# Optimization experiments

Measured on AMD Instinct MI355X. Metric: run time of the kernel, lower is better.

The kernel has to match this reference:

```python
import jax, jax.numpy as jnp
import numpy as np
from jax import lax


def _ln(x, g, b, eps=1e-5):
    m = jnp.mean(x, axis=-1, keepdims=True)
    v = jnp.mean((x - m) ** 2, axis=-1, keepdims=True)
    return (x - m) / jnp.sqrt(v + eps) * g + b


def _lin(x, w, b):  # torch Linear: w [out,in]
    return x @ w.T + b


def _conv(x, w, b, stride, pad):
    y = lax.conv_general_dilated(x, w, (stride, stride), pad,
                                 dimension_numbers=('NCHW', 'OIHW', 'NCHW'))
    return y + b[None, :, None, None]


def _haar_dwt(x):
    # J=1 haar, zero mode, even H/W: per 2x2 block [[a,b],[c,d]]
    a = x[:, :, 0::2, 0::2]
    bb = x[:, :, 0::2, 1::2]
    c = x[:, :, 1::2, 0::2]
    d = x[:, :, 1::2, 1::2]
    ll = (a + bb + c + d) * 0.5
    lohi = (a - bb + c - d) * 0.5  # band 0 (col-high)
    hilo = (a + bb - c - d) * 0.5  # band 1 (row-high)
    hihi = (a - bb - c + d) * 0.5  # band 2
    return ll, lohi, hilo, hihi


def _cross_attention(q, k, v):
    # q,k,v: [b, d, c]; 8 equal chunks along d; softmax over QUERY axis (torch dim=1)
    b, d, c = q.shape
    chunk = d // 8
    qc = q.reshape(b, 8, chunk, c)
    kc = k.reshape(b, 8, chunk, c)
    vc = v.reshape(b, 8, chunk, c)
    att = jnp.einsum('bnqc,bnkc->bnqk', qc, kc) * (8.0 ** -0.5)
    att = jax.nn.softmax(att, axis=2)  # normalize over q (matches F.softmax dim=1)
    out = jnp.einsum('bnqk,bnkc->bnqc', att, vc)
    return out.reshape(b, d, c)


def _ffn(x, ln1_g, ln1_b, fc1_w, fc1_b, div_w, div_b, fc2_w, fc2_b,
         ln3_g, ln3_b, fc3a_w, fc3a_b, fc3b_w, fc3b_b, lnn_g, lnn_b, act_w, act_b):
    x1 = jax.nn.gelu(_lin(_ln(x, ln1_g, ln1_b), fc1_w, fc1_b), approximate=False)
    x2 = jax.nn.gelu(_lin(x, div_w, div_b), approximate=False) - x1
    x2 = jax.nn.gelu(_lin(x2, fc2_w, fc2_b), approximate=False)
    x3 = _lin(jax.nn.gelu(_lin(_ln(x, ln3_g, ln3_b), fc3a_w, fc3a_b), approximate=False), fc3b_w, fc3b_b)
    gate = jax.nn.sigmoid(_lin(x, act_w, act_b))
    # dropout(0.5) is identity in eval mode
    return gate * _ln(x2 + x3, lnn_g, lnn_b)


def _resize_bilinear_ac(x, oh, ow):
    # bilinear, align_corners=True
    B, C, H, W = x.shape
    def idx(n_in, n_out):
        pos = jnp.linspace(0.0, n_in - 1.0, n_out)
        i0 = jnp.floor(pos).astype(jnp.int32)
        i1 = jnp.minimum(i0 + 1, n_in - 1)
        return i0, i1, (pos - i0).astype(x.dtype)
    y0, y1, wy = idx(H, oh)
    x0, x1, wx = idx(W, ow)
    r = x[:, :, y0, :] * (1 - wy)[None, None, :, None] + x[:, :, y1, :] * wy[None, None, :, None]
    return r[:, :, :, x0] * (1 - wx)[None, None, None, :] + r[:, :, :, x1] * wx[None, None, None, :]


def setup_inputs() -> dict:
    key = jax.random.key(0)
    ks = jax.random.split(key, 25)
    B, Cin, H, W = 16, 128, 128, 128
    Ch = 128  # out_planes // 2
    def nrm(k, shp, s=0.02):
        return jax.random.normal(k, shp, jnp.float32) * s
    inp = {
        'x': jax.random.normal(ks[0], (B, Cin, H, W), jnp.float32),
        'conv1_w': nrm(ks[1], (Ch, 2 * Cin, 1, 1)), 'conv1_b': jnp.zeros((Ch,), jnp.float32),
        'l1_w': nrm(ks[2], (Ch, Cin, 4, 4)), 'l1_b': jnp.zeros((Ch,), jnp.float32),
        'ln1_g': jnp.ones((Ch,), jnp.float32), 'ln1_b': jnp.zeros((Ch,), jnp.float32),
        'fc1_w': nrm(ks[3], (Ch, Ch)), 'fc1_b': jnp.zeros((Ch,), jnp.float32),
        'div_w': nrm(ks[4], (Ch, Ch)), 'div_b': jnp.zeros((Ch,), jnp.float32),
        'fc2_w': nrm(ks[5], (Ch, Ch)), 'fc2_b': jnp.zeros((Ch,), jnp.float32),
        'ln3_g': jnp.ones((Ch,), jnp.float32), 'ln3_b': jnp.zeros((Ch,), jnp.float32),
        'fc3a_w': nrm(ks[6], (Ch, Ch)), 'fc3a_b': jnp.zeros((Ch,), jnp.float32),
        'fc3b_w': nrm(ks[7], (Ch, Ch)), 'fc3b_b': jnp.zeros((Ch,), jnp.float32),
        'lnn_g': jnp.ones((Ch,), jnp.float32), 'lnn_b': jnp.zeros((Ch,), jnp.float32),
        'act_w': nrm(ks[8], (Ch, Ch)), 'act_b': jnp.zeros((Ch,), jnp.float32),
    }
    return inp


def reference(x, conv1_w, conv1_b, l1_w, l1_b, ln1_g, ln1_b, fc1_w, fc1_b,
              div_w, div_b, fc2_w, fc2_b, ln3_g, ln3_b, fc3a_w, fc3a_b,
              fc3b_w, fc3b_b, lnn_g, lnn_b, act_w, act_b):
    dw = jax.nn.relu(_conv(x, l1_w, l1_b, 2, ((1, 1), (1, 1))))
    yL, y_HL, y_LH, y_HH = _haar_dwt(x)
    y = _conv(jnp.concatenate((y_HL, y_LH), axis=1), conv1_w, conv1_b, 1, ((0, 0), (0, 0)))
    b, c, h, w = y.shape
    y_t = y.transpose(0, 2, 3, 1).reshape(b, h * w, c)
    yL_t = yL.transpose(0, 2, 3, 1).reshape(b, h * w, c)
    yHH_t = y_HH.transpose(0, 2, 3, 1).reshape(b, h * w, c)
    att = _cross_attention(yL_t, y_t, yHH_t)
    att = _ffn(att, ln1_g, ln1_b, fc1_w, fc1_b, div_w, div_b, fc2_w, fc2_b,
               ln3_g, ln3_b, fc3a_w, fc3a_b, fc3b_w, fc3b_b, lnn_g, lnn_b, act_w, act_b)
    att = att.reshape(b, h, w, c).transpose(0, 3, 1, 2)
    y_img = y_t.reshape(b, h, w, c).transpose(0, 3, 1, 2)
    down_2x = _resize_bilinear_ac(x, h, w)
    att = att * (down_2x - dw)
    return att + y_img
```

## Files before the change

kernel.cpp:

```cpp
#include <hip/hip_runtime.h>
#include <cmath>


#define EPI_NONE 0
#define EPI_GELU 1
#define EPI_GELU_SUB 2
#define EPI_ADD 3
#define EPI_SIGMOID 4
#define EPI_EXP 5

typedef unsigned short u16;
typedef __bf16 v8bf __attribute__((ext_vector_type(8)));
typedef float f32x4 __attribute__((ext_vector_type(4)));

__device__ __forceinline__ float gelu_f(float v) {
  return 0.5f * v * (1.f + erff(v * 0.70710678118654752f));
}
__device__ __forceinline__ float sigmoid_f(float v) {
  return 1.f / (1.f + __expf(-v));
}
__device__ __forceinline__ float bf2f(u16 h) {
  return __uint_as_float((unsigned)h << 16);
}
__device__ __forceinline__ u16 f2bf(float f) {
  unsigned u = __float_as_uint(f);
  return (u16)((u + 0x7fffu + ((u >> 16) & 1u)) >> 16);
}
__device__ __forceinline__ unsigned f2bf_pk(float lo, float hi) {
  unsigned a = __float_as_uint(lo), b = __float_as_uint(hi);
  a = (a + 0x7fffu + ((a >> 16) & 1u)) >> 16;
  b = (b + 0x7fffu + ((b >> 16) & 1u)) >> 16;
  return a | (b << 16);
}
__device__ __forceinline__ void gld_lds16(const void* g, void* l) {
  __builtin_amdgcn_global_load_lds(
      (const __attribute__((address_space(1))) unsigned int*)g,
      (__attribute__((address_space(3))) unsigned int*)l, 16, 0, 0);
}

__global__ __launch_bounds__(256) void pre_k(const float* __restrict__ x,
                                             u16* __restrict__ yL16,
                                             u16* __restrict__ yHHt16,
                                             u16* __restrict__ hllh16,
                                             u16* __restrict__ xpt) {
  int gx = blockIdx.x;
  int jt = gx & 1, cit = gx >> 1;
  int i = blockIdx.y, b = blockIdx.z;
  int j0 = jt * 32, ci0 = cit * 32;
  int tx = threadIdx.x & 31, ty = threadIdx.x >> 5;
  __shared__ float sll[32][33], shl[32][33], slh[32][33], shh[32][33];
  if (gx == 0) {
    int pl = 1 + ((threadIdx.x >> 7) << 1);
    long off = ((long)(b * 4 + pl) * 4160 + (long)i * 65) * 128 + (threadIdx.x & 127);
    xpt[off] = 0;
  } else if (gx == 1) {
    int pl = (threadIdx.x >> 7) << 1;
    long off = ((long)(b * 4 + pl) * 4160 + (long)i * 65 + 64) * 128 + (threadIdx.x & 127);
    xpt[off] = 0;
  }
  const float2* x2 = (const float2*)x;
#pragma unroll
  for (int k = 0; k < 4; ++k) {
    int ci = ty + 8 * k;
    long base = (((long)b * 128 + ci0 + ci) * 128 + 2 * i) * 64 + j0 + tx;
    float2 ab = x2[base];
    float2 cd = x2[base + 64];
    float a = ab.x, bb = ab.y, c = cd.x, d = cd.y;
    sll[ci][tx] = (a + bb + c + d) * 0.5f;
    shl[ci][tx] = (a - bb + c - d) * 0.5f;
    slh[ci][tx] = (a + bb - c - d) * 0.5f;
    shh[ci][tx] = (a - bb - c + d) * 0.5f;
  }
  __syncthreads();
  long tok = (long)b * 4096 + i * 64 + j0;
  int r = threadIdx.x >> 3;
  int q4 = (threadIdx.x & 7) << 2;
  float vll[4], vhl[4], vlh[4], vhh[4];
#pragma unroll
  for (int e = 0; e < 4; ++e) {
    vll[e] = sll[q4 + e][r];
    vhl[e] = shl[q4 + e][r];
    vlh[e] = slh[q4 + e][r];
    vhh[e] = shh[q4 + e][r];
  }
  uint2 u;
  u.x = f2bf_pk(vll[0], vll[1]);
  u.y = f2bf_pk(vll[2], vll[3]);
  *(uint2*)(yL16 + (tok + r) * 128 + ci0 + q4) = u;
  u.x = f2bf_pk(vhl[0], vhl[1]);
  u.y = f2bf_pk(vhl[2], vhl[3]);
  *(uint2*)(hllh16 + (tok + r) * 256 + ci0 + q4) = u;
  u.x = f2bf_pk(vlh[0], vlh[1]);
  u.y = f2bf_pk(vlh[2], vlh[3]);
  *(uint2*)(hllh16 + (tok + r) * 256 + 128 + ci0 + q4) = u;
  {
    int ch = threadIdx.x >> 3;
    int t4 = (threadIdx.x & 7) << 2;
    uint2 h;
    h.x = f2bf_pk(shh[ch][t4], shh[ch][t4 + 1]);
    h.y = f2bf_pk(shh[ch][t4 + 2], shh[ch][t4 + 3]);
    *(uint2*)(yHHt16 + (long)(ci0 + ch) * 65536 + tok + t4) = h;
  }
  {
    long rb = (long)(b * 4) * 4160 + (long)i * 65;
    int ci = j0 + r;
    float pA[4], pB[4], pC[4], pD[4];
#pragma unroll
    for (int e = 0; e < 4; ++e) {
      pA[e] = 0.5f * (vll[e] + vhl[e] + vlh[e] + vhh[e]);
      pB[e] = 0.5f * (vll[e] - vhl[e] + vlh[e] - vhh[e]);
      pC[e] = 0.5f * (vll[e] + vhl[e] - vlh[e] - vhh[e]);
      pD[e] = 0.5f * (vll[e] - vhl[e] - vlh[e] + vhh[e]);
    }
    u.x = f2bf_pk(pA[0], pA[1]);
    u.y = f2bf_pk(pA[2], pA[3]);
    *(uint2*)(xpt + (rb + ci) * 128 + ci0 + q4) = u;
    u.x = f2bf_pk(pB[0], pB[1]);
    u.y = f2bf_pk(pB[2], pB[3]);
    *(uint2*)(xpt + (rb + 4160 + ci + 1) * 128 + ci0 + q4) = u;
    u.x = f2bf_pk(pC[0], pC[1]);
    u.y = f2bf_pk(pC[2], pC[3]);
    *(uint2*)(xpt + (rb + 8320 + ci) * 128 + ci0 + q4) = u;
    u.x = f2bf_pk(pD[0], pD[1]);
    u.y = f2bf_pk(pD[2], pD[3]);
    *(uint2*)(xpt + (rb + 12480 + ci + 1) * 128 + ci0 + q4) = u;
  }
}

__global__ __launch_bounds__(256) void wcvt8_k(
    const float* __restrict__ a0, const float* __restrict__ a1,
    const float* __restrict__ a2, const float* __restrict__ a3,
    const float* __restrict__ a4, const float* __restrict__ a5,
    const float* __restrict__ a6, const float* __restrict__ a7,
    unsigned* __restrict__ dst, unsigned* __restrict__ zp) {
  if (blockIdx.x >= 768) {
    zp[(blockIdx.x - 768) * 256 + threadIdx.x] = 0;
    return;
  }
  int f = blockIdx.x * 256 + threadIdx.x;
  int e = 2 * f;
  if (e < 262144) {
    int ch = e >> 13, kg = (e >> 10) & 7, n = (e >> 3) & 127, ke = e & 7;
    int k = ch * 64 + kg * 8 + ke;
    int stg = ch >> 2, sub = ch & 3;
    int kwsel = sub >> 1, chalf = sub & 1;
    int kh = stg >> 1, cp = stg & 1;
    int kw = cp ? (kwsel ? 2 : 0) : (kwsel ? 3 : 1);
    int c = chalf * 64 + (k & 63);
    long si = (((long)n * 128 + c) * 4 + kh) * 4 + kw;
    dst[f] = f2bf_pk(a0[si], a0[si + 16]);
    return;
  }
  const float* s; int b;
  if (e < 294912)      { s = a1; b = 262144; }
  else if (e < 311296) { s = a2; b = 294912; }
  else if (e < 327680) { s = a3; b = 311296; }
  else if (e < 344064) { s = a4; b = 327680; }
  else if (e < 360448) { s = a5; b = 344064; }
  else if (e < 376832) { s = a6; b = 360448; }
  else                 { s = a7; b = 376832; }
  dst[f] = f2bf_pk(s[e - b], s[e - b + 1]);
}

template <int AMODE, int EPI>
__global__ __launch_bounds__(256) void gemm16_k(
    const u16* __restrict__ A, long sA, int lda,
    const u16* __restrict__ B, long sB, int ldb,
    u16* __restrict__ C, long sC, int ldc,
    int K, float alpha, const float* __restrict__ bias,
    const u16* __restrict__ aux, const float* __restrict__ sc) {
  __shared__ __align__(16) char smem[32768];
  char* As = smem;
  char* Bs = smem + 16384;
  int z = blockIdx.z;
  int tid = threadIdx.x, lane = tid & 63, w = tid >> 6;
  int wm = w >> 1, wn = w & 1, l15 = lane & 15, l4 = lane >> 4;
  const u16* Ab = A + (long)z * sA + (long)blockIdx.x * 128 * lda;
  const u16* Bb = B + (long)z * sB + (long)blockIdx.y * 128 * ldb;
  const float* scz = (AMODE == 1) ? sc + (long)z * K : nullptr;
  int sm = tid >> 3, skg = tid & 7;
  int sbase = sm * 128 + ((skg ^ (sm & 7)) << 4);
  uint4 pa[4], pb[4];

  auto loadAB = [&](int k0) {
#pragma unroll
    for (int u = 0; u < 4; ++u) {
      pb[u] = *(const uint4*)(Bb + (long)(sm + 32 * u) * ldb + k0 + skg * 8);
      uint4 v = *(const uint4*)(Ab + (long)(sm + 32 * u) * lda + k0 + skg * 8);
      if (AMODE == 1) {
        float4 s0 = *(const float4*)(scz + k0 + skg * 8);
        float4 s1 = *(const float4*)(scz + k0 + skg * 8 + 4);
        v.x = f2bf_pk(bf2f((u16)(v.x & 0xffff)) * s0.x, bf2f((u16)(v.x >> 16)) * s0.y);
        v.y = f2bf_pk(bf2f((u16)(v.y & 0xffff)) * s0.z, bf2f((u16)(v.y >> 16)) * s0.w);
        v.z = f2bf_pk(bf2f((u16)(v.z & 0xffff)) * s1.x, bf2f((u16)(v.z >> 16)) * s1.y);
        v.w = f2bf_pk(bf2f((u16)(v.w & 0xffff)) * s1.z, bf2f((u16)(v.w >> 16)) * s1.w);
      }
      pa[u] = v;
    }
  };

  f32x4 acc[4][4] = {};
  loadAB(0);
  int nch = K >> 6;
  for (int ch = 0; ch < nch; ++ch) {
    __syncthreads();
#pragma unroll
    for (int u = 0; u < 4; ++u) {
      *(uint4*)(As + sbase + u * 4096) = pa[u];
      *(uint4*)(Bs + sbase + u * 4096) = pb[u];
    }
    __syncthreads();
    if (ch + 1 < nch) loadAB((ch + 1) << 6);
#pragma unroll
    for (int s = 0; s < 2; ++s) {
      int ko = (((s << 2) | l4) ^ (l15 & 7)) << 4;
      v8bf af[4], bfr[4];
#pragma unroll
      for (int t = 0; t < 4; ++t) {
        af[t] = *(const v8bf*)(As + (64 * wm + 16 * t + l15) * 128 + ko);
        bfr[t] = *(const v8bf*)(Bs + (64 * wn + 16 * t + l15) * 128 + ko);
      }
#pragma unroll
      for (int mt = 0; mt < 4; ++mt)
#pragma unroll
        for (int nt = 0; nt < 4; ++nt)
          acc[mt][nt] = __builtin_amdgcn_mfma_f32_16x16x32_bf16(af[mt], bfr[nt], acc[mt][nt], 0, 0, 0);
    }
  }
  u16* Cb = C + (long)z * sC;
#pragma unroll
  for (int mt = 0; mt < 4; ++mt) {
#pragma unroll
    for (int nt = 0; nt < 4; ++nt) {
      f32x4 a = acc[mt][nt];
      int n = blockIdx.y * 128 + 64 * wn + 16 * nt + l15;
      float bv = bias ? bias[n] : 0.f;
#pragma unroll
      for (int r = 0; r < 4; ++r) {
        long m = (long)blockIdx.x * 128 + 64 * wm + 16 * mt + 4 * l4 + r;
        float v = a[r] * alpha + bv;
        if (EPI == EPI_GELU) v = gelu_f(v);
        else if (EPI == EPI_GELU_SUB) v = gelu_f(v) - bf2f(aux[m * ldc + n]);
        else if (EPI == EPI_ADD) v += bf2f(aux[m * ldc + n]);
        else if (EPI == EPI_SIGMOID) v = sigmoid_f(v);
        else if (EPI == EPI_EXP) v = __expf(v);
        Cb[m * ldc + n] = f2bf(v);
      }
    }
  }
}

__global__ __launch_bounds__(256) __attribute__((amdgpu_waves_per_eu(4)))
void conv4g_k(const u16* __restrict__ xpt, const u16* __restrict__ wb,
              const float* __restrict__ bias, const u16* __restrict__ zp,
              u16* __restrict__ dw16) {
  __shared__ __align__(16) char smem[33280];
  char* As = smem;
  int raw = blockIdx.x;
  int swz = (raw & 7) * 128 + (raw >> 3);
  int oi = swz & 63, b = swz >> 6;
  int tid = threadIdx.x, lane = tid & 63, w = tid >> 6;
  int wm = w >> 1, wn = w & 1, l15 = lane & 15, l4 = lane >> 4;
  f32x4 acc[2][4] = {};

  auto issueA = [&](int stg2, int bsel) {
    int kh = stg2 >> 1, cp2 = stg2 & 1;
    int roff = (kh == 0) ? -1 : (kh == 3) ? 1 : 0;
    int ri = oi + roff;
    int ph = (((kh + 1) & 1) << 1) | cp2;
    const u16* rowb = ((unsigned)ri < 64u)
        ? xpt + ((long)(b * 4 + ph) * 4160 + (long)ri * 65) * 128
        : zp;
    char* lb = As + bsel * 16640 + w * 1024;
#pragma unroll
    for (int i = 0; i < 4; ++i) {
      int d = i * 4096 + w * 1024 + lane * 16;
      int slot = d >> 8, cg = (d >> 4) & 15;
      gld_lds16(rowb + slot * 128 + ((cg ^ ((slot - cp2) & 7)) << 3),
                lb + i * 4096);
    }
    if (tid < 16) {
      gld_lds16(rowb + 64 * 128 + ((lane ^ ((64 - cp2) & 7)) << 3),
                As + bsel * 16640 + 16384);
    }
  };

  issueA(0, 0);
  for (int stg = 0; stg < 8; ++stg) {
    __syncthreads();
    if (stg < 7) issueA(stg + 1, (stg + 1) & 1);
    const char* Ab = As + (stg & 1) * 16640;
    int cp2 = stg & 1;
#pragma unroll
    for (int sub = 0; sub < 4; ++sub) {
      int chunk = stg * 4 + sub;
      const int kwsel = sub >> 1, chalf = sub & 1;
#pragma unroll
      for (int s = 0; s < 2; ++s) {
        v8bf bw[4], af[2];
#pragma unroll
        for (int nt = 0; nt < 4; ++nt) {
          int row = 64 * wn + 16 * nt + l15;
          bw[nt] = *(const v8bf*)(wb + ((long)(chunk * 8 + s * 4 + l4) * 128 + row) * 8);
        }
#pragma unroll
        for (int mt = 0; mt < 2; ++mt) {
          int slot = 32 * wm + 16 * mt + l15 + kwsel;
          int cg = chalf * 8 + s * 4 + l4;
          af[mt] = *(const v8bf*)(Ab + slot * 256 + ((cg ^ ((slot - cp2) & 7)) << 4));
        }
#pragma unroll
        for (int mt = 0; mt < 2; ++mt)
#pragma unroll
          for (int nt = 0; nt < 4; ++nt)
            acc[mt][nt] = __builtin_amdgcn_mfma_f32_16x16x32_bf16(
                af[mt], bw[nt], acc[mt][nt], 0, 0, 0);
      }
    }
  }
  __syncthreads();
  float* buf = (float*)(smem + w * 2176);
  long obase = ((long)b * 128) * 4096 + oi * 64;
#pragma unroll
  for (int cg = 0; cg < 4; ++cg) {
    int co = 64 * wn + 16 * cg + l15;
    float bv = bias[co];
#pragma unroll
    for (int mt = 0; mt < 2; ++mt) {
      f32x4 a = acc[mt][cg];
#pragma unroll
      for (int r = 0; r < 4; ++r)
        buf[l15 * 34 + 16 * mt + 4 * l4 + r] = fmaxf(a[r] + bv, 0.f);
    }
    __syncthreads();
#pragma unroll
    for (int it = 0; it < 8; ++it) {
      int row = it * 2 + (lane >> 5);
      int mcol = lane & 31;
      int coz = 64 * wn + 16 * cg + row;
      dw16[obase + (long)coz * 4096 + 32 * wm + mcol] = f2bf(buf[row * 34 + mcol]);
    }
    __syncthreads();
  }
}

__global__ __launch_bounds__(256) void ssum_k(const u16* __restrict__ E,
                                              float* __restrict__ sc) {
  int z = blockIdx.y;
  int k = blockIdx.x * 256 + threadIdx.x;
  const u16* Eb = E + (long)z * 262144 + k;
  float s = 0.f;
#pragma unroll 8
  for (int q = 0; q < 512; ++q) s += bf2f(Eb[(long)q * 512]);
  sc[(long)z * 512 + k] = 1.f / s;
}

__global__ __launch_bounds__(256) void ln16_k(const u16* __restrict__ X,
                                              const float* __restrict__ g,
                                              const float* __restrict__ bt,
                                              const u16* __restrict__ gate,
                                              u16* __restrict__ Y) {
  int t = (blockIdx.x * 256 + threadIdx.x) >> 6;
  int lane = threadIdx.x & 63;
  const u16* xr = X + (long)t * 128;
  float v0 = bf2f(xr[lane]), v1 = bf2f(xr[lane + 64]);
  float s = v0 + v1, sq = v0 * v0 + v1 * v1;
#pragma unroll
  for (int off = 32; off > 0; off >>= 1) {
    s += __shfl_xor(s, off);
    sq += __shfl_xor(sq, off);
  }
  float mean = s * 0.0078125f;
  float var = sq * 0.0078125f - mean * mean;
  float rstd = rsqrtf(var + 1e-5f);
  float y0 = (v0 - mean) * rstd * g[lane] + bt[lane];
  float y1 = (v1 - mean) * rstd * g[lane + 64] + bt[lane + 64];
  if (gate) {
    y0 *= bf2f(gate[(long)t * 128 + lane]);
    y1 *= bf2f(gate[(long)t * 128 + lane + 64]);
  }
  Y[(long)t * 128 + lane] = f2bf(y0);
  Y[(long)t * 128 + lane + 64] = f2bf(y1);
}

__global__ __launch_bounds__(256) void combine_k(const u16* __restrict__ attf,
                                                 const u16* __restrict__ yt,
                                                 const u16* __restrict__ dw16,
                                                 const float* __restrict__ x,
                                                 float* __restrict__ out) {
  int gx = blockIdx.x;
  int jt = gx & 1, cot = gx >> 1;
  int i = blockIdx.y, b = blockIdx.z;
  int j0 = jt * 32, co0 = cot * 32;
  int tx = threadIdx.x & 31, ty = threadIdx.x >> 5;
  __shared__ float sa[32][33], sy[32][33];
  long tokbase = (long)b * 4096 + i * 64 + j0;
#pragma unroll
  for (int k = 0; k < 4; ++k) {
    int row = ty + 8 * k;
    long idx = (tokbase + row) * 128 + co0 + tx;
    sa[row][tx] = bf2f(attf[idx]);
    sy[row][tx] = bf2f(yt[idx]);
  }
  __syncthreads();
  float py = (float)(i * 127) / 63.0f;
  int y0 = (int)py;
  int y1 = min(y0 + 1, 127);
  float wy = py - (float)y0;
  int j = j0 + tx;
  float px = (float)(j * 127) / 63.0f;
  int x0 = (int)px;
  int x1 = min(x0 + 1, 127);
  float wx = px - (float)x0;
#pragma unroll
  for (int k = 0; k < 4; ++k) {
    int co = co0 + ty + 8 * k;
    const float* xb = x + (((long)b * 128 + co) * 128) * 128;
    float r0 = xb[y0 * 128 + x0] * (1.f - wx) + xb[y0 * 128 + x1] * wx;
    float r1 = xb[y1 * 128 + x0] * (1.f - wx) + xb[y1 * 128 + x1] * wx;
    float d2 = r0 * (1.f - wy) + r1 * wy;
    long oidx = (((long)b * 128 + co) * 64 + i) * 64 + j;
    float dwv = bf2f(dw16[oidx]);
    out[oidx] = sa[tx][ty + 8 * k] * (d2 - dwv) + sy[tx][ty + 8 * k];
  }
}

extern "C" void kernel_launch(void* const* d_in, const int* in_sizes, int n_in,
                              void* d_out, int out_size, void* d_ws, size_t ws_size,
                              hipStream_t stream) {
  const float* x = (const float*)d_in[0];
  const float* w1 = (const float*)d_in[1];
  const float* b1 = (const float*)d_in[2];
  const float* l1w = (const float*)d_in[3];
  const float* l1b = (const float*)d_in[4];
  const float* ln1g = (const float*)d_in[5];
  const float* ln1b = (const float*)d_in[6];
  const float* fc1w = (const float*)d_in[7];
  const float* fc1b = (const float*)d_in[8];
  const float* divw = (const float*)d_in[9];
  const float* divb = (const float*)d_in[10];
  const float* fc2w = (const float*)d_in[11];
  const float* fc2b = (const float*)d_in[12];
  const float* ln3g = (const float*)d_in[13];
  const float* ln3b = (const float*)d_in[14];
  const float* fc3aw = (const float*)d_in[15];
  const float* fc3ab = (const float*)d_in[16];
  const float* fc3bw = (const float*)d_in[17];
  const float* fc3bb = (const float*)d_in[18];
  const float* lnng = (const float*)d_in[19];
  const float* lnnb = (const float*)d_in[20];
  const float* actw = (const float*)d_in[21];
  const float* actb = (const float*)d_in[22];

  char* W = (char*)d_ws;
  u16* yL16 = (u16*)(W);
  u16* hllh16 = (u16*)(W + 16777216L);
  u16* yHHt16 = (u16*)(W + 50331648L);
  u16* y16 = (u16*)(W + 67108864L);
  u16* S16 = (u16*)(W + 83886080L);
  u16* attO16 = (u16*)(W + 150994944L);
  u16* dw16 = (u16*)(W + 167772160L);
  u16* t1 = (u16*)(W + 184549376L);
  u16* t2 = (u16*)(W + 201326592L);
  u16* t3 = (u16*)(W + 218103808L);
  u16* t4 = (u16*)(W + 234881024L);
  float* sc = (float*)(W + 251658240L);
  u16* wall = (u16*)(W + 251920384L);
  u16* l1wb = wall;
  u16* w1b = wall + 262144;
  u16* fc1b16 = wall + 294912;
  u16* divb16 = wall + 311296;
  u16* fc2b16 = wall + 327680;
  u16* fc3ab16 = wall + 344064;
  u16* fc3bb16 = wall + 360448;
  u16* actb16 = wall + 376832;
  u16* xpt16 = S16;
  u16* zp16 = (u16*)(W + 152043520L);

  dim3 blk(256);
  const float qk_scale = 0.35355339059327373f;

  wcvt8_k<<<dim3(785), blk, 0, stream>>>(l1w, w1, fc1w, divw, fc2w, fc3aw,
                                         fc3bw, actw, (unsigned*)wall,
                                         (unsigned*)zp16);
  pre_k<<<dim3(8, 64, 16), blk, 0, stream>>>(x, yL16, yHHt16, hllh16, xpt16);
  gemm16_k<0, EPI_NONE><<<dim3(512, 1, 1), blk, 0, stream>>>(
      hllh16, 0, 256, w1b, 0, 256, y16, 0, 128, 256, 1.f, b1, nullptr, nullptr);
  conv4g_k<<<dim3(1024), blk, 0, stream>>>(xpt16, l1wb, l1b, zp16, dw16);
  gemm16_k<0, EPI_EXP><<<dim3(4, 4, 128), blk, 0, stream>>>(
      yL16, 65536, 128, y16, 65536, 128, S16, 262144, 512, 128, qk_scale,
      nullptr, nullptr, nullptr);
  ssum_k<<<dim3(2, 128), blk, 0, stream>>>(S16, sc);
  gemm16_k<1, EPI_NONE><<<dim3(4, 1, 128), blk, 0, stream>>>(
      S16, 262144, 512, yHHt16, 512, 65536, attO16, 65536, 128, 512, 1.f,
      nullptr, nullptr, sc);
  ln16_k<<<16384, blk, 0, stream>>>(attO16, ln1g, ln1b, nullptr, t1);
  gemm16_k<0, EPI_GELU><<<dim3(512, 1, 1), blk, 0, stream>>>(
      t1, 0, 128, fc1b16, 0, 128, t2, 0, 128, 128, 1.f, fc1b, nullptr, nullptr);
  gemm16_k<0, EPI_GELU_SUB><<<dim3(512, 1, 1), blk, 0, stream>>>(
      attO16, 0, 128, divb16, 0, 128, t3, 0, 128, 128, 1.f, divb, t2, nullptr);
  gemm16_k<0, EPI_GELU><<<dim3(512, 1, 1), blk, 0, stream>>>(
      t3, 0, 128, fc2b16, 0, 128, t4, 0, 128, 128, 1.f, fc2b, nullptr, nullptr);
  ln16_k<<<16384, blk, 0, stream>>>(attO16, ln3g, ln3b, nullptr, t1);
  gemm16_k<0, EPI_GELU><<<dim3(512, 1, 1), blk, 0, stream>>>(
      t1, 0, 128, fc3ab16, 0, 128, t3, 0, 128, 128, 1.f, fc3ab, nullptr, nullptr);
  gemm16_k<0, EPI_ADD><<<dim3(512, 1, 1), blk, 0, stream>>>(
      t3, 0, 128, fc3bb16, 0, 128, t1, 0, 128, 128, 1.f, fc3bb, t4, nullptr);
  gemm16_k<0, EPI_SIGMOID><<<dim3(512, 1, 1), blk, 0, stream>>>(
      attO16, 0, 128, actb16, 0, 128, t3, 0, 128, 128, 1.f, actb, nullptr, nullptr);
  ln16_k<<<16384, blk, 0, stream>>>(t1, lnng, lnnb, t3, t2);
  combine_k<<<dim3(8, 64, 16), blk, 0, stream>>>(t2, y16, dw16, x, (float*)d_out);
}
```

Before: 663.4 us.

## Fuse entire FFN block (layernorms, six GEMMs, epilogues) into one kernel

Replaces nine separate launches (three layernorm kernels and six small GEMMs with epilogues) with a single kernel. Each block loads a 64-token tile into LDS and runs every layernorm, matmul and activation on chip. Only the final gated layernorm output goes back to global memory. This removes the round trips of intermediate activations through HBM and the launch overhead. In exchange it adds many block-wide barriers, reads weights straight from global or cache in every block, and runs with lower per-block GEMM parallelism.

Result: faster. 610.0 us (-8.0%).

```diff
diff --git a/kernel.cpp b/kernel.cpp
--- a/kernel.cpp
+++ b/kernel.cpp
@@ -3,10 +3,6 @@
 
 
 #define EPI_NONE 0
-#define EPI_GELU 1
-#define EPI_GELU_SUB 2
-#define EPI_ADD 3
-#define EPI_SIGMOID 4
 #define EPI_EXP 5
 
 typedef unsigned short u16;
@@ -239,13 +235,184 @@
       for (int r = 0; r < 4; ++r) {
         long m = (long)blockIdx.x * 128 + 64 * wm + 16 * mt + 4 * l4 + r;
         float v = a[r] * alpha + bv;
-        if (EPI == EPI_GELU) v = gelu_f(v);
-        else if (EPI == EPI_GELU_SUB) v = gelu_f(v) - bf2f(aux[m * ldc + n]);
-        else if (EPI == EPI_ADD) v += bf2f(aux[m * ldc + n]);
-        else if (EPI == EPI_SIGMOID) v = sigmoid_f(v);
-        else if (EPI == EPI_EXP) v = __expf(v);
+        if (EPI == EPI_EXP) v = __expf(v);
         Cb[m * ldc + n] = f2bf(v);
       }
+    }
+  }
+}
+
+__global__ __launch_bounds__(256) void ffn_k(
+    const u16* __restrict__ Xg,
+    const u16* __restrict__ w_fc1, const u16* __restrict__ w_div,
+    const u16* __restrict__ w_fc2, const u16* __restrict__ w_fc3a,
+    const u16* __restrict__ w_fc3b, const u16* __restrict__ w_act,
+    const float* __restrict__ b_fc1, const float* __restrict__ b_div,
+    const float* __restrict__ b_fc2, const float* __restrict__ b_fc3a,
+    const float* __restrict__ b_fc3b, const float* __restrict__ b_act,
+    const float* __restrict__ ln1g, const float* __restrict__ ln1b,
+    const float* __restrict__ ln3g, const float* __restrict__ ln3b,
+    const float* __restrict__ lnng, const float* __restrict__ lnnb,
+    u16* __restrict__ out) {
+  __shared__ __align__(16) char smem[49152];
+  char* X = smem;
+  char* A = smem + 16384;
+  char* E = smem + 32768;
+  int z = blockIdx.x;
+  long t0 = (long)z * 64;
+  int tid = threadIdx.x, lane = tid & 63, w = tid >> 6;
+  int wm = w >> 1, wn = w & 1, l15 = lane & 15, l4 = lane >> 4;
+
+  {
+    const u16* src = Xg + t0 * 128;
+#pragma unroll
+    for (int r = 0; r < 4; ++r) {
+      int u = r * 256 + tid;
+      int row = u >> 4, cg = u & 15;
+      gld_lds16(src + row * 128 + ((cg ^ (row & 7)) << 3),
+                X + (r * 256 + w * 64) * 16);
+    }
+  }
+
+  auto gemm = [&](const char* Asrc, const u16* Bg, f32x4 (&acc)[2][4]) {
+#pragma unroll
+    for (int mt = 0; mt < 2; ++mt)
+#pragma unroll
+      for (int nt = 0; nt < 4; ++nt) acc[mt][nt] = f32x4{0.f, 0.f, 0.f, 0.f};
+#pragma unroll
+    for (int s = 0; s < 4; ++s) {
+      v8bf af[2], bw[4];
+#pragma unroll
+      for (int mt = 0; mt < 2; ++mt) {
+        int row = 32 * wm + 16 * mt + l15;
+        af[mt] = *(const v8bf*)(Asrc + row * 256 + (((s * 4 + l4) ^ (row & 7)) << 4));
+      }
+#pragma unroll
+      for (int nt = 0; nt < 4; ++nt) {
+        int rn = 64 * wn + 16 * nt + l15;
+        bw[nt] = *(const v8bf*)(Bg + rn * 128 + (s * 4 + l4) * 8);
+      }
+#pragma unroll
+      for (int mt = 0; mt < 2; ++mt)
+#pragma unroll
+        for (int nt = 0; nt < 4; ++nt)
+          acc[mt][nt] = __builtin_amdgcn_mfma_f32_16x16x32_bf16(
+              af[mt], bw[nt], acc[mt][nt], 0, 0, 0);
+    }
+  };
+
+  auto epi = [&](f32x4 (&acc)[2][4], const float* bias, char* dst,
+                 const char* Eb, int mode) {
+#pragma unroll
+    for (int nt = 0; nt < 4; ++nt) {
+      int n = 64 * wn + 16 * nt + l15;
+      float bv = bias[n];
+#pragma unroll
+      for (int mt = 0; mt < 2; ++mt) {
+#pragma unroll
+        for (int r = 0; r < 4; ++r) {
+          int m = 32 * wm + 16 * mt + 4 * l4 + r;
+          int off = m * 256 + (((n >> 3) ^ (m & 7)) << 4) + (n & 7) * 2;
+          float v = acc[mt][nt][r] + bv;
+          if (mode == 0) v = gelu_f(v);
+          else if (mode == 1) v = gelu_f(v) - bf2f(*(const u16*)(Eb + off));
+          else if (mode == 2) v += bf2f(*(const u16*)(Eb + off));
+          else v = sigmoid_f(v);
+          *(u16*)(dst + off) = f2bf(v);
+        }
+      }
+    }
+  };
+
+  auto lnpass = [&](const char* src, char* dst, const float* g,
+                    const float* bt) {
+    int row = w * 16 + (lane >> 2), q = lane & 3;
+    float v[32];
+    float s = 0.f, sq = 0.f;
+#pragma unroll
+    for (int gi = 0; gi < 4; ++gi) {
+      int gr = q * 4 + gi;
+      v8bf hv = *(const v8bf*)(src + row * 256 + ((gr ^ (row & 7)) << 4));
+#pragma unroll
+      for (int e = 0; e < 8; ++e) {
+        float f = bf2f(((const u16*)&hv)[e]);
+        v[gi * 8 + e] = f;
+        s += f;
+        sq += f * f;
+      }
+    }
+    s += __shfl_xor(s, 1); sq += __shfl_xor(sq, 1);
+    s += __shfl_xor(s, 2); sq += __shfl_xor(sq, 2);
+    float mean = s * 0.0078125f;
+    float rstd = rsqrtf(sq * 0.0078125f - mean * mean + 1e-5f);
+#pragma unroll
+    for (int gi = 0; gi < 4; ++gi) {
+      int gr = q * 4 + gi;
+      int c0 = gr * 8;
+      unsigned o[4];
+#pragma unroll
+      for (int e = 0; e < 4; ++e) {
+        float y0 = (v[gi * 8 + 2 * e] - mean) * rstd * g[c0 + 2 * e] + bt[c0 + 2 * e];
+        float y1 = (v[gi * 8 + 2 * e + 1] - mean) * rstd * g[c0 + 2 * e + 1] + bt[c0 + 2 * e + 1];
+        o[e] = f2bf_pk(y0, y1);
+      }
+      *(uint4*)(dst + row * 256 + ((gr ^ (row & 7)) << 4)) = *(uint4*)o;
+    }
+  };
+
+  f32x4 acc[2][4];
+  __syncthreads();
+  lnpass(X, A, ln1g, ln1b); __syncthreads();
+  gemm(A, w_fc1, acc); __syncthreads();
+  epi(acc, b_fc1, E, nullptr, 0); __syncthreads();
+  gemm(X, w_div, acc); __syncthreads();
+  epi(acc, b_div, A, E, 1); __syncthreads();
+  gemm(A, w_fc2, acc); __syncthreads();
+  epi(acc, b_fc2, E, nullptr, 0); __syncthreads();
+  lnpass(X, A, ln3g, ln3b); __syncthreads();
+  gemm(A, w_fc3a, acc); __syncthreads();
+  epi(acc, b_fc3a, A, nullptr, 0); __syncthreads();
+  gemm(A, w_fc3b, acc); __syncthreads();
+  epi(acc, b_fc3b, A, E, 2); __syncthreads();
+  gemm(X, w_act, acc); __syncthreads();
+  epi(acc, b_act, E, nullptr, 3); __syncthreads();
+
+  {
+    int row = w * 16 + (lane >> 2), q = lane & 3;
+    float v[32];
+    float s = 0.f, sq = 0.f;
+#pragma unroll
+    for (int gi = 0; gi < 4; ++gi) {
+      int gr = q * 4 + gi;
+      v8bf hv = *(const v8bf*)(A + row * 256 + ((gr ^ (row & 7)) << 4));
+#pragma unroll
+      for (int e = 0; e < 8; ++e) {
+        float f = bf2f(((const u16*)&hv)[e]);
+        v[gi * 8 + e] = f;
+        s += f;
+        sq += f * f;
+      }
+    }
+    s += __shfl_xor(s, 1); sq += __shfl_xor(sq, 1);
+    s += __shfl_xor(s, 2); sq += __shfl_xor(sq, 2);
+    float mean = s * 0.0078125f;
+    float rstd = rsqrtf(sq * 0.0078125f - mean * mean + 1e-5f);
+    u16* og = out + (t0 + row) * 128;
+#pragma unroll
+    for (int gi = 0; gi < 4; ++gi) {
+      int gr = q * 4 + gi;
+      int c0 = gr * 8;
+      v8bf gv = *(const v8bf*)(E + row * 256 + ((gr ^ (row & 7)) << 4));
+      unsigned o[4];
+#pragma unroll
+      for (int e = 0; e < 4; ++e) {
+        float y0 = ((v[gi * 8 + 2 * e] - mean) * rstd * lnng[c0 + 2 * e] + lnnb[c0 + 2 * e]) *
+                   bf2f(((const u16*)&gv)[2 * e]);
+        float y1 = ((v[gi * 8 + 2 * e + 1] - mean) * rstd * lnng[c0 + 2 * e + 1] + lnnb[c0 + 2 * e + 1]) *
+                   bf2f(((const u16*)&gv)[2 * e + 1]);
+        o[e] = f2bf_pk(y0, y1);
+      }
+      *(uint4*)(og + c0) = *(uint4*)o;
     }
   }
 }
@@ -353,34 +520,6 @@
 #pragma unroll 8
   for (int q = 0; q < 512; ++q) s += bf2f(Eb[(long)q * 512]);
   sc[(long)z * 512 + k] = 1.f / s;
-}
-
-__global__ __launch_bounds__(256) void ln16_k(const u16* __restrict__ X,
-                                              const float* __restrict__ g,
-                                              const float* __restrict__ bt,
-                                              const u16* __restrict__ gate,
-                                              u16* __restrict__ Y) {
-  int t = (blockIdx.x * 256 + threadIdx.x) >> 6;
-  int lane = threadIdx.x & 63;
-  const u16* xr = X + (long)t * 128;
-  float v0 = bf2f(xr[lane]), v1 = bf2f(xr[lane + 64]);
-  float s = v0 + v1, sq = v0 * v0 + v1 * v1;
-#pragma unroll
-  for (int off = 32; off > 0; off >>= 1) {
-    s += __shfl_xor(s, off);
-    sq += __shfl_xor(sq, off);
-  }
-  float mean = s * 0.0078125f;
-  float var = sq * 0.0078125f - mean * mean;
-  float rstd = rsqrtf(var + 1e-5f);
-  float y0 = (v0 - mean) * rstd * g[lane] + bt[lane];
-  float y1 = (v1 - mean) * rstd * g[lane + 64] + bt[lane + 64];
-  if (gate) {
-    y0 *= bf2f(gate[(long)t * 128 + lane]);
-    y1 *= bf2f(gate[(long)t * 128 + lane + 64]);
-  }
-  Y[(long)t * 128 + lane] = f2bf(y0);
-  Y[(long)t * 128 + lane + 64] = f2bf(y1);
 }
 
 __global__ __launch_bounds__(256) void combine_k(const u16* __restrict__ attf,
@@ -460,10 +599,7 @@
   u16* S16 = (u16*)(W + 83886080L);
   u16* attO16 = (u16*)(W + 150994944L);
   u16* dw16 = (u16*)(W + 167772160L);
-  u16* t1 = (u16*)(W + 184549376L);
   u16* t2 = (u16*)(W + 201326592L);
-  u16* t3 = (u16*)(W + 218103808L);
-  u16* t4 = (u16*)(W + 234881024L);
   float* sc = (float*)(W + 251658240L);
   u16* wall = (u16*)(W + 251920384L);
   u16* l1wb = wall;
@@ -494,20 +630,9 @@
   gemm16_k<1, EPI_NONE><<<dim3(4, 1, 128), blk, 0, stream>>>(
       S16, 262144, 512, yHHt16, 512, 65536, attO16, 65536, 128, 512, 1.f,
       nullptr, nullptr, sc);
-  ln16_k<<<16384, blk, 0, stream>>>(attO16, ln1g, ln1b, nullptr, t1);
-  gemm16_k<0, EPI_GELU><<<dim3(512, 1, 1), blk, 0, stream>>>(
-      t1, 0, 128, fc1b16, 0, 128, t2, 0, 128, 128, 1.f, fc1b, nullptr, nullptr);
-  gemm16_k<0, EPI_GELU_SUB><<<dim3(512, 1, 1), blk, 0, stream>>>(
-      attO16, 0, 128, divb16, 0, 128, t3, 0, 128, 128, 1.f, divb, t2, nullptr);
-  gemm16_k<0, EPI_GELU><<<dim3(512, 1, 1), blk, 0, stream>>>(
-      t3, 0, 128, fc2b16, 0, 128, t4, 0, 128, 128, 1.f, fc2b, nullptr, nullptr);
-  ln16_k<<<16384, blk, 0, stream>>>(attO16, ln3g, ln3b, nullptr, t1);
-  gemm16_k<0, EPI_GELU><<<dim3(512, 1, 1), blk, 0, stream>>>(
-      t1, 0, 128, fc3ab16, 0, 128, t3, 0, 128, 128, 1.f, fc3ab, nullptr, nullptr);
-  gemm16_k<0, EPI_ADD><<<dim3(512, 1, 1), blk, 0, stream>>>(
-      t3, 0, 128, fc3bb16, 0, 128, t1, 0, 128, 128, 1.f, fc3bb, t4, nullptr);
-  gemm16_k<0, EPI_SIGMOID><<<dim3(512, 1, 1), blk, 0, stream>>>(
-      attO16, 0, 128, actb16, 0, 128, t3, 0, 128, 128, 1.f, actb, nullptr, nullptr);
-  ln16_k<<<16384, blk, 0, stream>>>(t1, lnng, lnnb, t3, t2);
+  ffn_k<<<dim3(1024), blk, 0, stream>>>(
+      attO16, fc1b16, divb16, fc2b16, fc3ab16, fc3bb16, actb16,
+      fc1b, divb, fc2b, fc3ab, fc3bb, actb,
+      ln1g, ln1b, ln3g, ln3b, lnng, lnnb, t2);
   combine_k<<<dim3(8, 64, 16), blk, 0, stream>>>(t2, y16, dw16, x, (float*)d_out);
 }
```
